# Performance work log

Hardware: AMD Instinct MI355X
Metric: run time of the kernel (lower is better)

The kernel has to match this reference:

```python
import jax, jax.numpy as jnp
import numpy as np

VOL = (32, 64, 64)          # 3D brain volume grid
B, N, D = 2, 4096, 1024     # batch, active voxels (seq_len), feature_dim
H, KNN = 16, 16             # num_heads, num_neighbors


def setup_inputs() -> dict:
    key = jax.random.key(0)
    k1, k2, k3, k4 = jax.random.split(key, 4)
    # boolean 3D mask with exactly N active voxels (so seq_len == #active)
    rng = np.random.default_rng(0)
    flat = np.zeros(int(np.prod(VOL)), dtype=bool)
    flat[rng.choice(flat.size, N, replace=False)] = True
    visual_cortex_mask = jnp.asarray(flat.reshape(VOL))
    x = jax.random.normal(k1, (B, N, D), dtype=jnp.float32)
    s = 1.0 / np.sqrt(D)
    Wq = jax.random.normal(k2, (D, D), dtype=jnp.float32) * s
    Wk = jax.random.normal(k3, (D, D), dtype=jnp.float32) * s
    Wv = jax.random.normal(k4, (D, D), dtype=jnp.float32) * s
    return {"x": x, "visual_cortex_mask": visual_cortex_mask,
            "Wq": Wq, "Wk": Wk, "Wv": Wv}


def reference(x, visual_cortex_mask, Wq, Wk, Wv):
    batch, seq_len, d = x.shape
    hd = d // H
    # --- kNN over active voxel coordinates (cdist + topk) ---
    flat = visual_cortex_mask.reshape(-1)
    (act,) = jnp.nonzero(flat, size=seq_len)  # flat indices of active voxels
    coords = jnp.stack(jnp.unravel_index(act, visual_cortex_mask.shape),
                       axis=1).astype(jnp.float32)           # [N, 3]
    sq = jnp.sum(coords * coords, axis=-1)                    # [N]
    d2 = sq[:, None] + sq[None, :] - 2.0 * (coords @ coords.T)  # squared dists
    _, nbr = jax.lax.top_k(-d2, KNN + 1)   # smallest distances first
    nbr = nbr[:, 1:]                       # drop self -> [N, KNN] positions
    # --- QKV projections (torch Linear: x @ W.T) ---
    q = (x @ Wq.T).reshape(batch, seq_len, H, hd)
    k = (x @ Wk.T).reshape(batch, seq_len, H, hd)
    v = (x @ Wv.T).reshape(batch, seq_len, H, hd)
    # --- gather-based sparse attention: each query attends only to its
    # KNN neighbors (exactly the block-mask semantics of the original) ---
    kn = k[:, nbr]   # [B, N, KNN, H, hd]
    vn = v[:, nbr]   # [B, N, KNN, H, hd]
    scale = 1.0 / np.sqrt(hd)
    scores = jnp.einsum('bnhd,bnkhd->bhnk', q, kn) * scale
    attn = jax.nn.softmax(scores, axis=-1)
    out = jnp.einsum('bhnk,bnkhd->bnhd', attn, vn).reshape(batch, seq_len, d)
    metric = k.mean(axis=2)  # key.mean over heads -> [B, N, hd]
    return out, metric
```

## Files before the change

### kernel.cpp

```cpp
#include <hip/hip_runtime.h>
#include <hip/hip_bf16.h>
#include <stdint.h>

#define BATCH 2
#define NPTS 4096
#define DMODEL 1024
#define NHEAD 16
#define HDIM 64
#define KNN 16
#define MASKN 131072
#define EBLK 128

typedef __attribute__((ext_vector_type(8))) short bf16x8;
typedef __attribute__((ext_vector_type(4))) float f32x4;

__device__ __forceinline__ float b2f(unsigned short u) {
    union { unsigned int i; float f; } c; c.i = ((unsigned int)u) << 16; return c.f;
}
__device__ __forceinline__ unsigned short f2b(float f) {
    unsigned int x = __float_as_uint(f);
    unsigned int r = (x + 0x7fffu + ((x >> 16) & 1u)) >> 16;
    return (unsigned short)r;
}
__device__ __forceinline__ unsigned int pack2f(float a, float b) {
    return (unsigned int)f2b(a) | ((unsigned int)f2b(b) << 16);
}
__device__ __forceinline__ void gload16(const unsigned short* g, unsigned short* l) {
    __builtin_amdgcn_global_load_lds((const __attribute__((address_space(1))) void*)g,
                                     (__attribute__((address_space(3))) void*)l, 16, 0, 0);
}

__global__ __launch_bounds__(256) void count8_kernel(const unsigned char* __restrict__ m8,
                                                     int* __restrict__ cnt8) {
    __shared__ int red[256];
    const int b = blockIdx.x, t = threadIdx.x;
    const uchar4 v = ((const uchar4*)m8)[b * 256 + t];
    red[t] = (v.x != 0) + (v.y != 0) + (v.z != 0) + (v.w != 0);
    __syncthreads();
    for (int off = 128; off >= 1; off >>= 1) {
        if (t < off) red[t] += red[t + off];
        __syncthreads();
    }
    if (t == 0) cnt8[b] = red[0];
}

__global__ __launch_bounds__(256) void count32_kernel(const unsigned char* __restrict__ m8,
                                                      const int* __restrict__ cnt8,
                                                      int* __restrict__ cnt32) {
    __shared__ int red[256];
    const int b = blockIdx.x, t = threadIdx.x;
    red[t] = (t < EBLK) ? cnt8[t] : 0;
    __syncthreads();
    for (int off = 128; off >= 1; off >>= 1) {
        if (t < off) red[t] += red[t + off];
        __syncthreads();
    }
    if (red[0] == NPTS) return;
    __syncthreads();
    const int4 v = ((const int4*)m8)[b * 256 + t];
    red[t] = (v.x != 0) + (v.y != 0) + (v.z != 0) + (v.w != 0);
    __syncthreads();
    for (int off = 128; off >= 1; off >>= 1) {
        if (t < off) red[t] += red[t + off];
        __syncthreads();
    }
    if (t == 0) cnt32[b] = red[0];
}

__global__ __launch_bounds__(256) void extract_kernel(const unsigned char* __restrict__ m8,
                                                      const int* __restrict__ cnt8,
                                                      const int* __restrict__ cnt32,
                                                      int* __restrict__ act) {
    __shared__ int sblk[EBLK];
    __shared__ int sthr[256];
    const int b = blockIdx.x, t = threadIdx.x;
    if (t < EBLK) sblk[t] = cnt8[t];
    __syncthreads();
    for (int off = 1; off < EBLK; off <<= 1) {
        int v = (t < EBLK && t >= off) ? sblk[t - off] : 0;
        __syncthreads();
        if (t < EBLK) sblk[t] += v;
        __syncthreads();
    }
    const bool bytes = (sblk[EBLK - 1] == NPTS);
    if (!bytes) {
        __syncthreads();
        if (t < EBLK) sblk[t] = cnt32[t];
        __syncthreads();
        for (int off = 1; off < EBLK; off <<= 1) {
            int v = (t < EBLK && t >= off) ? sblk[t - off] : 0;
            __syncthreads();
            if (t < EBLK) sblk[t] += v;
            __syncthreads();
        }
    }
    const int blkoff = (b == 0) ? 0 : sblk[b - 1];
    const int gbase = b * 1024 + t * 4;
    int f0, f1, f2, f3;
    if (bytes) {
        const uchar4 v = ((const uchar4*)m8)[b * 256 + t];
        f0 = v.x != 0; f1 = v.y != 0; f2 = v.z != 0; f3 = v.w != 0;
    } else {
        const int4 v = ((const int4*)m8)[b * 256 + t];
        f0 = v.x != 0; f1 = v.y != 0; f2 = v.z != 0; f3 = v.w != 0;
    }
    const int c = f0 + f1 + f2 + f3;
    sthr[t] = c;
    __syncthreads();
    for (int off = 1; off < 256; off <<= 1) {
        int v = (t >= off) ? sthr[t - off] : 0;
        __syncthreads();
        sthr[t] += v;
        __syncthreads();
    }
    int pos = blkoff + sthr[t] - c;
    if (f0) act[pos++] = gbase;
    if (f1) act[pos++] = gbase + 1;
    if (f2) act[pos++] = gbase + 2;
    if (f3) act[pos++] = gbase + 3;
}

__global__ __launch_bounds__(256) void knn_kernel(const int* __restrict__ act,
                                                  int* __restrict__ nbr) {
    __shared__ int act_s[NPTS];
    const int t = threadIdx.x;
    for (int i = t; i < NPTS; i += 256) act_s[i] = act[i];
    __syncthreads();
    const int q = blockIdx.x * 4 + (t >> 6);
    const int lane = t & 63;
    const int aq = act_s[q];
    const int qz = aq >> 12, qy = (aq >> 6) & 63, qx = aq & 63;
    int best[17];
    #pragma unroll
    for (int i = 0; i < 17; ++i) best[i] = 0x7FFFFFFF;
    for (int j = lane; j < NPTS; j += 64) {
        const int aj = act_s[j];
        const int dz = (aj >> 12) - qz;
        const int dy = ((aj >> 6) & 63) - qy;
        const int dx = (aj & 63) - qx;
        const int d2 = dz * dz + dy * dy + dx * dx;
        int p = (d2 << 12) | j;
        if (p < best[16]) {
            #pragma unroll
            for (int u = 0; u < 17; ++u) {
                const bool lt = p < best[u];
                const int tmp = best[u];
                best[u] = lt ? p : best[u];
                p = lt ? tmp : p;
            }
        }
    }
    int head = best[0];
    int keep = 0;
    #pragma unroll
    for (int r = 0; r < KNN + 1; ++r) {
        int m = head;
        #pragma unroll
        for (int off = 32; off >= 1; off >>= 1) m = min(m, __shfl_xor(m, off, 64));
        if (lane == r - 1) keep = m;
        const bool win = (head == m);
        #pragma unroll
        for (int u = 0; u < 16; ++u) if (win) best[u] = best[u + 1];
        if (win) best[16] = 0x7FFFFFFF;
        head = best[0];
    }
    if (lane < KNN) nbr[q * KNN + lane] = keep & 4095;
}

#define XN8 (BATCH * NPTS * DMODEL / 8)
#define WN8 (DMODEL * DMODEL / 8)
__global__ __launch_bounds__(256) void cast_all_kernel(
    const float* __restrict__ x, const float* __restrict__ wq,
    const float* __restrict__ wk, const float* __restrict__ wv,
    unsigned short* __restrict__ Xb, unsigned short* __restrict__ Wb) {
    const int i = blockIdx.x * 256 + threadIdx.x;
    const int total = XN8 + 3 * WN8;
    if (i >= total) return;
    const float* src;
    unsigned short* dst;
    if (i < XN8) {
        src = x + (size_t)i * 8;
        dst = Xb + (size_t)i * 8;
    } else {
        const int j = i - XN8;
        const int wsel = j >> 17;
        const int o = j & (WN8 - 1);
        src = ((wsel == 0) ? wq : (wsel == 1) ? wk : wv) + (size_t)o * 8;
        dst = Wb + ((size_t)wsel * WN8 + o) * 8;
    }
    const float4 a = ((const float4*)src)[0];
    const float4 b = ((const float4*)src)[1];
    uint4 w;
    w.x = pack2f(a.x, a.y); w.y = pack2f(a.z, a.w);
    w.z = pack2f(b.x, b.y); w.w = pack2f(b.z, b.w);
    *(uint4*)dst = w;
}

__global__ __launch_bounds__(256, 2) void gemm_qkv64(
    const unsigned short* __restrict__ Xb,
    const unsigned short* __restrict__ Wb,
    unsigned short* __restrict__ O0, unsigned short* __restrict__ O1, unsigned short* __restrict__ O2)
{
    const int K = DMODEL, N = DMODEL;
    const unsigned short* W = Wb + (size_t)blockIdx.z * DMODEL * DMODEL;
    unsigned short* C = (blockIdx.z == 0) ? O0 : (blockIdx.z == 1) ? O1 : O2;
    __shared__ unsigned short As[2][128 * 64];
    __shared__ unsigned short Bs[2][128 * 64];
    const int tid = threadIdx.x;
    const int rowBase = blockIdx.x * 128;
    const int colBase = blockIdx.y * 128;
    const int lane = tid & 63, w = tid >> 6;
    const int wr = w >> 1, wc = w & 1;
    const int lr = lane & 15, kg = lane >> 4;

    f32x4 acc[4][4];
    const f32x4 zero = {0.f, 0.f, 0.f, 0.f};
    #pragma unroll
    for (int i = 0; i < 4; ++i)
        #pragma unroll
        for (int j = 0; j < 4; ++j) acc[i][j] = zero;

    const unsigned short* aS[4];
    const unsigned short* bS[4];
    #pragma unroll
    for (int j = 0; j < 4; ++j) {
        const int s = j * 256 + tid;
        const int row = s >> 3, pch = s & 7;
        const int sc = (pch ^ (row & 7)) * 8;
        aS[j] = Xb + (size_t)(rowBase + row) * K + sc;
        bS[j] = W  + (size_t)(colBase + row) * K + sc;
    }

    #define STAGE(kt, bf) do { \
        _Pragma("unroll") \
        for (int j = 0; j < 4; ++j) { \
            gload16(aS[j] + (kt) * 64, &As[bf][(j * 256 + w * 64) * 8]); \
            gload16(bS[j] + (kt) * 64, &Bs[bf][(j * 256 + w * 64) * 8]); \
        } \
    } while (0)

    #define COMPUTE(bf) do { \
        bf16x8 af[4][2], bfr[4][2]; \
        _Pragma("unroll") \
        for (int mi = 0; mi < 4; ++mi) \
            _Pragma("unroll") \
            for (int kk = 0; kk < 2; ++kk) \
                af[mi][kk] = *(const bf16x8*)&As[bf][(wr * 64 + mi * 16 + lr) * 64 + (((kk * 4 + kg) ^ (lr & 7)) * 8)]; \
        _Pragma("unroll") \
        for (int ni = 0; ni < 4; ++ni) \
            _Pragma("unroll") \
            for (int kk = 0; kk < 2; ++kk) \
                bfr[ni][kk] = *(const bf16x8*)&Bs[bf][(wc * 64 + ni * 16 + lr) * 64 + (((kk * 4 + kg) ^ (lr & 7)) * 8)]; \
        __builtin_amdgcn_s_setprio(1); \
        _Pragma("unroll") \
        for (int kk = 0; kk < 2; ++kk) \
            _Pragma("unroll") \
            for (int mi = 0; mi < 4; ++mi) \
                _Pragma("unroll") \
                for (int ni = 0; ni < 4; ++ni) \
                    acc[mi][ni] = __builtin_amdgcn_mfma_f32_16x16x32_bf16(af[mi][kk], bfr[ni][kk], acc[mi][ni], 0, 0, 0); \
        __builtin_amdgcn_s_setprio(0); \
    } while (0)

    STAGE(0, 0);
    STAGE(1, 1);
    for (int kt = 0; kt < 14; ++kt) {
        const int bf = kt & 1;
        asm volatile("s_waitcnt vmcnt(8)" ::: "memory");
        __builtin_amdgcn_s_barrier();
        COMPUTE(bf);
        __builtin_amdgcn_s_barrier();
        STAGE(kt + 2, bf);
    }
    asm volatile("s_waitcnt vmcnt(8)" ::: "memory");
    __builtin_amdgcn_s_barrier();
    COMPUTE(0);
    __builtin_amdgcn_s_barrier();
    asm volatile("s_waitcnt vmcnt(0)" ::: "memory");
    __builtin_amdgcn_s_barrier();
    COMPUTE(1);
    #undef STAGE
    #undef COMPUTE

    #pragma unroll
    for (int mi = 0; mi < 4; ++mi)
        #pragma unroll
        for (int ni = 0; ni < 4; ++ni) {
            const int row0 = rowBase + wr * 64 + mi * 16 + kg * 4;
            const int col = colBase + wc * 64 + ni * 16 + lr;
            #pragma unroll
            for (int j = 0; j < 4; ++j)
                C[(size_t)(row0 + j) * N + col] = f2b(acc[mi][ni][j]);
        }
}

__device__ __forceinline__ void stage16(unsigned short* dst, const float* src) {
    const float4 a = ((const float4*)src)[0];
    const float4 b = ((const float4*)src)[1];
    const float4 c = ((const float4*)src)[2];
    const float4 d = ((const float4*)src)[3];
    uint4 w0, w1;
    w0.x = pack2f(a.x, a.y); w0.y = pack2f(a.z, a.w);
    w0.z = pack2f(b.x, b.y); w0.w = pack2f(b.z, b.w);
    w1.x = pack2f(c.x, c.y); w1.y = pack2f(c.z, c.w);
    w1.z = pack2f(d.x, d.y); w1.w = pack2f(d.z, d.w);
    ((uint4*)dst)[0] = w0;
    ((uint4*)dst)[1] = w1;
}

__global__ __launch_bounds__(256) void gemm_qkv_f32(
    const float* __restrict__ X,
    const float* __restrict__ W0, const float* __restrict__ W1, const float* __restrict__ W2,
    unsigned short* __restrict__ O0, unsigned short* __restrict__ O1, unsigned short* __restrict__ O2)
{
    const int K = DMODEL, N = DMODEL;
    const float* W = (blockIdx.z == 0) ? W0 : (blockIdx.z == 1) ? W1 : W2;
    unsigned short* C = (blockIdx.z == 0) ? O0 : (blockIdx.z == 1) ? O1 : O2;
    __shared__ unsigned short As[128 * 32];
    __shared__ unsigned short Bs[128 * 32];
    const int tid = threadIdx.x;
    const int rowBase = blockIdx.x * 128;
    const int colBase = blockIdx.y * 128;
    const int lane = tid & 63, w = tid >> 6;
    const int wr = w >> 1, wc = w & 1;
    const int lr = lane & 15, kg = lane >> 4;
    const int srow = tid >> 1;
    const int scol = (tid & 1) * 16;
    f32x4 acc[4][4];
    const f32x4 zero = {0.f, 0.f, 0.f, 0.f};
    #pragma unroll
    for (int i = 0; i < 4; ++i)
        #pragma unroll
        for (int j = 0; j < 4; ++j) acc[i][j] = zero;
    const float* Arow = &X[(size_t)(rowBase + srow) * K + scol];
    const float* Brow = &W[(size_t)(colBase + srow) * K + scol];
    unsigned short* Adst = &As[srow * 32 + scol];
    unsigned short* Bdst = &Bs[srow * 32 + scol];
    for (int kb = 0; kb < K; kb += 32) {
        __syncthreads();
        stage16(Adst, Arow + kb);
        stage16(Bdst, Brow + kb);
        __syncthreads();
        bf16x8 af[4], bfr[4];
        #pragma unroll
        for (int mi = 0; mi < 4; ++mi)
            af[mi] = *(const bf16x8*)&As[(wr * 64 + mi * 16 + lr) * 32 + kg * 8];
        #pragma unroll
        for (int ni = 0; ni < 4; ++ni)
            bfr[ni] = *(const bf16x8*)&Bs[(wc * 64 + ni * 16 + lr) * 32 + kg * 8];
        #pragma unroll
        for (int mi = 0; mi < 4; ++mi)
            #pragma unroll
            for (int ni = 0; ni < 4; ++ni)
                acc[mi][ni] = __builtin_amdgcn_mfma_f32_16x16x32_bf16(af[mi], bfr[ni], acc[mi][ni], 0, 0, 0);
    }
    #pragma unroll
    for (int mi = 0; mi < 4; ++mi)
        #pragma unroll
        for (int ni = 0; ni < 4; ++ni) {
            const int row0 = rowBase + wr * 64 + mi * 16 + kg * 4;
            const int col = colBase + wc * 64 + ni * 16 + lr;
            #pragma unroll
            for (int j = 0; j < 4; ++j)
                C[(size_t)(row0 + j) * N + col] = f2b(acc[mi][ni][j]);
        }
}

__global__ __launch_bounds__(256) void attn_kernel(
    const unsigned short* __restrict__ Q, const unsigned short* __restrict__ Kb,
    const unsigned short* __restrict__ Vb, const int* __restrict__ nbr,
    float* __restrict__ out, float* __restrict__ mout)
{
    const int bid = blockIdx.x;
    const int p = (bid & 7) * 1024 + (bid >> 3);
    const int b = p >> 12;
    const int n = p & 4095;
    __shared__ unsigned short q_s[DMODEL];
    __shared__ float a_s[NHEAD][KNN];
    __shared__ float part_s[4][64];
    const int tid = threadIdx.x;
    const int kk = tid & 15, h = tid >> 4;
    const int mynb = nbr[n * KNN + kk];
    const unsigned short* krow = &Kb[((size_t)b * NPTS + mynb) * DMODEL + h * HDIM];
    bf16x8 kreg[8];
    #pragma unroll
    for (int j = 0; j < 8; ++j) kreg[j] = *(const bf16x8*)&krow[j * 8];
    const int o = tid * 4;
    ushort4 vpre[KNN];
    #pragma unroll
    for (int k2 = 0; k2 < KNN; ++k2) {
        const int nb2 = __shfl(mynb, k2, 16);
        vpre[k2] = *(const ushort4*)&Vb[((size_t)b * NPTS + nb2) * DMODEL + o];
    }
    *(int2*)&q_s[tid * 4] = *(const int2*)&Q[((size_t)b * NPTS + n) * DMODEL + tid * 4];
    __syncthreads();
    float s = 0.f;
    #pragma unroll
    for (int j = 0; j < 8; ++j) {
        const bf16x8 qq = *(const bf16x8*)&q_s[h * HDIM + j * 8];
        const bf16x8 kr = kreg[j];
        #pragma unroll
        for (int e = 0; e < 8; ++e)
            s += b2f((unsigned short)qq[e]) * b2f((unsigned short)kr[e]);
    }
    s *= 0.125f;
    float m = s;
    #pragma unroll
    for (int off = 8; off >= 1; off >>= 1) m = fmaxf(m, __shfl_xor(m, off, 16));
    const float e = __expf(s - m);
    float sum = e;
    #pragma unroll
    for (int off = 8; off >= 1; off >>= 1) sum += __shfl_xor(sum, off, 16);
    a_s[h][kk] = e / sum;
    __syncthreads();
    const int h2 = tid >> 4;
    float av0 = 0.f, av1 = 0.f, av2 = 0.f, av3 = 0.f;
    #pragma unroll
    for (int k2 = 0; k2 < KNN; ++k2) {
        const float a = a_s[h2][k2];
        av0 += a * b2f(vpre[k2].x); av1 += a * b2f(vpre[k2].y);
        av2 += a * b2f(vpre[k2].z); av3 += a * b2f(vpre[k2].w);
    }
    float4 r; r.x = av0; r.y = av1; r.z = av2; r.w = av3;
    *(float4*)&out[((size_t)b * NPTS + n) * DMODEL + o] = r;
    {
        const unsigned short* krow2 = &Kb[((size_t)b * NPTS + n) * DMODEL];
        const int dd = tid & 63, grp = tid >> 6;
        float ms = 0.f;
        #pragma unroll
        for (int hh = 0; hh < 4; ++hh)
            ms += b2f(krow2[(grp * 4 + hh) * HDIM + dd]);
        part_s[grp][dd] = ms;
        __syncthreads();
        if (tid < 64)
            mout[((size_t)b * NPTS + n) * HDIM + tid] =
                (part_s[0][tid] + part_s[1][tid] + part_s[2][tid] + part_s[3][tid]) * 0.0625f;
    }
}

extern "C" void kernel_launch(void* const* d_in, const int* in_sizes, int n_in,
                              void* d_out, int out_size, void* d_ws, size_t ws_size,
                              hipStream_t stream) {
    const float* x = (const float*)d_in[0];
    const unsigned char* mask = (const unsigned char*)d_in[1];
    const float* Wq = (const float*)d_in[2];
    const float* Wk = (const float*)d_in[3];
    const float* Wv = (const float*)d_in[4];
    float* out = (float*)d_out;
    char* ws = (char*)d_ws;

    const size_t QKV_BYTES = (size_t)BATCH * NPTS * DMODEL * 2;
    const size_t XB_BYTES  = (size_t)BATCH * NPTS * DMODEL * 2;
    const size_t WB_BYTES  = (size_t)3 * DMODEL * DMODEL * 2;
    unsigned short* qb = (unsigned short*)(ws);
    unsigned short* kb = (unsigned short*)(ws + QKV_BYTES);
    unsigned short* vb = (unsigned short*)(ws + 2 * QKV_BYTES);
    const size_t SMALL_BYTES = (size_t)NPTS * sizeof(int) * (1 + KNN) + 2 * EBLK * sizeof(int);
    const size_t need_base = 3 * QKV_BYTES + SMALL_BYTES;
    const size_t need_full = need_base + XB_BYTES + WB_BYTES;
    const bool full = (ws_size >= need_full);
    char* tail = ws + 3 * QKV_BYTES;
    unsigned short* Xb = (unsigned short*)tail;
    unsigned short* Wb = (unsigned short*)(tail + XB_BYTES);
    char* small = full ? (tail + XB_BYTES + WB_BYTES) : tail;
    int* act  = (int*)small;
    int* nbr  = (int*)(small + NPTS * sizeof(int));
    int* cnt8 = (int*)(small + NPTS * sizeof(int) * (1 + KNN));
    int* cnt32 = cnt8 + EBLK;
    if (ws_size < need_base) return;

    count8_kernel<<<EBLK, 256, 0, stream>>>(mask, cnt8);
    count32_kernel<<<EBLK, 256, 0, stream>>>(mask, cnt8, cnt32);
    extract_kernel<<<EBLK, 256, 0, stream>>>(mask, cnt8, cnt32, act);
    knn_kernel<<<1024, 256, 0, stream>>>(act, nbr);
    if (full) {
        const int castN = XN8 + 3 * WN8;
        cast_all_kernel<<<(castN + 255) / 256, 256, 0, stream>>>(x, Wq, Wk, Wv, Xb, Wb);
        gemm_qkv64<<<dim3(64, 8, 3), 256, 0, stream>>>(Xb, Wb, qb, kb, vb);
    } else {
        gemm_qkv_f32<<<dim3(64, 8, 3), 256, 0, stream>>>(x, Wq, Wk, Wv, qb, kb, vb);
    }
    attn_kernel<<<dim3(BATCH * NPTS), 256, 0, stream>>>(qb, kb, vb, nbr, out,
                                                        out + (size_t)BATCH * NPTS * DMODEL);
}
```

Measured before the change: 174.4 us.

## Merge mask count/extract kernels and co-launch kNN with bf16 cast

The three mask-processing kernels (count8, count32, extract) are replaced by one prep kernel in which every block redundantly counts the whole mask to compute its prefix offset. The kNN search and the fp32-to-bf16 cast are merged into one launch, with block ranges split by blockIdx, so the two independent jobs can run at the same time. The aim is fewer launches and less idle tail between small kernels. In exchange each prep block rereads the full mask, and the kNN blocks now reserve 16KB of shared memory per block even in the cast path.

Result: slower. 180.6 us (+3.5%).

```diff
diff --git a/kernel.cpp b/kernel.cpp
--- a/kernel.cpp
+++ b/kernel.cpp
@@ -9,7 +9,6 @@
 #define HDIM 64
 #define KNN 16
 #define MASKN 131072
-#define EBLK 128
 
 typedef __attribute__((ext_vector_type(8))) short bf16x8;
 typedef __attribute__((ext_vector_type(4))) float f32x4;
@@ -30,78 +29,55 @@
                                      (__attribute__((address_space(3))) void*)l, 16, 0, 0);
 }
 
-__global__ __launch_bounds__(256) void count8_kernel(const unsigned char* __restrict__ m8,
-                                                     int* __restrict__ cnt8) {
-    __shared__ int red[256];
-    const int b = blockIdx.x, t = threadIdx.x;
-    const uchar4 v = ((const uchar4*)m8)[b * 256 + t];
-    red[t] = (v.x != 0) + (v.y != 0) + (v.z != 0) + (v.w != 0);
-    __syncthreads();
-    for (int off = 128; off >= 1; off >>= 1) {
-        if (t < off) red[t] += red[t + off];
-        __syncthreads();
-    }
-    if (t == 0) cnt8[b] = red[0];
-}
-
-__global__ __launch_bounds__(256) void count32_kernel(const unsigned char* __restrict__ m8,
-                                                      const int* __restrict__ cnt8,
-                                                      int* __restrict__ cnt32) {
-    __shared__ int red[256];
-    const int b = blockIdx.x, t = threadIdx.x;
-    red[t] = (t < EBLK) ? cnt8[t] : 0;
-    __syncthreads();
-    for (int off = 128; off >= 1; off >>= 1) {
-        if (t < off) red[t] += red[t + off];
-        __syncthreads();
-    }
-    if (red[0] == NPTS) return;
-    __syncthreads();
-    const int4 v = ((const int4*)m8)[b * 256 + t];
-    red[t] = (v.x != 0) + (v.y != 0) + (v.z != 0) + (v.w != 0);
-    __syncthreads();
-    for (int off = 128; off >= 1; off >>= 1) {
-        if (t < off) red[t] += red[t + off];
-        __syncthreads();
-    }
-    if (t == 0) cnt32[b] = red[0];
-}
-
-__global__ __launch_bounds__(256) void extract_kernel(const unsigned char* __restrict__ m8,
-                                                      const int* __restrict__ cnt8,
-                                                      const int* __restrict__ cnt32,
-                                                      int* __restrict__ act) {
-    __shared__ int sblk[EBLK];
+__global__ __launch_bounds__(256) void prep_kernel(const unsigned char* __restrict__ m8,
+                                                   int* __restrict__ act) {
     __shared__ int sthr[256];
     const int b = blockIdx.x, t = threadIdx.x;
-    if (t < EBLK) sblk[t] = cnt8[t];
+    int cnt = 0;
+    const uchar4* v8 = (const uchar4*)m8;
+    for (int i = 0; i < 128; ++i) {
+        const uchar4 v = v8[t * 128 + i];
+        cnt += (v.x != 0) + (v.y != 0) + (v.z != 0) + (v.w != 0);
+    }
+    sthr[t] = cnt;
     __syncthreads();
-    for (int off = 1; off < EBLK; off <<= 1) {
-        int v = (t < EBLK && t >= off) ? sblk[t - off] : 0;
-        __syncthreads();
-        if (t < EBLK) sblk[t] += v;
-        __syncthreads();
-    }
-    const bool bytes = (sblk[EBLK - 1] == NPTS);
-    if (!bytes) {
-        __syncthreads();
-        if (t < EBLK) sblk[t] = cnt32[t];
-        __syncthreads();
-        for (int off = 1; off < EBLK; off <<= 1) {
-            int v = (t < EBLK && t >= off) ? sblk[t - off] : 0;
+    for (int off = 1; off < 256; off <<= 1) {
+        int v = (t >= off) ? sthr[t - off] : 0;
+        __syncthreads();
+        sthr[t] += v;
+        __syncthreads();
+    }
+    const bool bytes = (sthr[255] == NPTS);
+    int blkoff;
+    if (bytes) {
+        blkoff = (b == 0) ? 0 : sthr[2 * b - 1];
+        __syncthreads();
+    } else {
+        __syncthreads();
+        const int4* v32 = (const int4*)m8;
+        int c2 = 0;
+        for (int i = 0; i < 128; ++i) {
+            const int4 v = v32[t * 128 + i];
+            c2 += (v.x != 0) + (v.y != 0) + (v.z != 0) + (v.w != 0);
+        }
+        sthr[t] = c2;
+        __syncthreads();
+        for (int off = 1; off < 256; off <<= 1) {
+            int v = (t >= off) ? sthr[t - off] : 0;
             __syncthreads();
-            if (t < EBLK) sblk[t] += v;
+            sthr[t] += v;
             __syncthreads();
         }
-    }
-    const int blkoff = (b == 0) ? 0 : sblk[b - 1];
+        blkoff = (b == 0) ? 0 : sthr[2 * b - 1];
+        __syncthreads();
+    }
     const int gbase = b * 1024 + t * 4;
     int f0, f1, f2, f3;
     if (bytes) {
-        const uchar4 v = ((const uchar4*)m8)[b * 256 + t];
+        const uchar4 v = ((const uchar4*)m8)[gbase >> 2];
         f0 = v.x != 0; f1 = v.y != 0; f2 = v.z != 0; f3 = v.w != 0;
     } else {
-        const int4 v = ((const int4*)m8)[b * 256 + t];
+        const int4 v = ((const int4*)m8)[gbase >> 2];
         f0 = v.x != 0; f1 = v.y != 0; f2 = v.z != 0; f3 = v.w != 0;
     }
     const int c = f0 + f1 + f2 + f3;
@@ -120,80 +96,83 @@
     if (f3) act[pos++] = gbase + 3;
 }
 
-__global__ __launch_bounds__(256) void knn_kernel(const int* __restrict__ act,
-                                                  int* __restrict__ nbr) {
+#define XN8 (BATCH * NPTS * DMODEL / 8)
+#define WN8 (DMODEL * DMODEL / 8)
+#define CASTN (XN8 + 3 * WN8)
+#define CASTBLKS ((CASTN + 255) / 256)
+
+__global__ __launch_bounds__(256) void knn_cast_kernel(
+    const int* __restrict__ act, int* __restrict__ nbr,
+    const float* __restrict__ x, const float* __restrict__ wq,
+    const float* __restrict__ wk, const float* __restrict__ wv,
+    unsigned short* __restrict__ Xb, unsigned short* __restrict__ Wb)
+{
     __shared__ int act_s[NPTS];
     const int t = threadIdx.x;
-    for (int i = t; i < NPTS; i += 256) act_s[i] = act[i];
-    __syncthreads();
-    const int q = blockIdx.x * 4 + (t >> 6);
-    const int lane = t & 63;
-    const int aq = act_s[q];
-    const int qz = aq >> 12, qy = (aq >> 6) & 63, qx = aq & 63;
-    int best[17];
-    #pragma unroll
-    for (int i = 0; i < 17; ++i) best[i] = 0x7FFFFFFF;
-    for (int j = lane; j < NPTS; j += 64) {
-        const int aj = act_s[j];
-        const int dz = (aj >> 12) - qz;
-        const int dy = ((aj >> 6) & 63) - qy;
-        const int dx = (aj & 63) - qx;
-        const int d2 = dz * dz + dy * dy + dx * dx;
-        int p = (d2 << 12) | j;
-        if (p < best[16]) {
+    if (blockIdx.x < 1024) {
+        for (int i = t; i < NPTS; i += 256) act_s[i] = act[i];
+        __syncthreads();
+        const int q = blockIdx.x * 4 + (t >> 6);
+        const int lane = t & 63;
+        const int aq = act_s[q];
+        const int qz = aq >> 12, qy = (aq >> 6) & 63, qx = aq & 63;
+        int best[17];
+        #pragma unroll
+        for (int i = 0; i < 17; ++i) best[i] = 0x7FFFFFFF;
+        for (int j = lane; j < NPTS; j += 64) {
+            const int aj = act_s[j];
+            const int dz = (aj >> 12) - qz;
+            const int dy = ((aj >> 6) & 63) - qy;
+            const int dx = (aj & 63) - qx;
+            const int d2 = dz * dz + dy * dy + dx * dx;
+            int p = (d2 << 12) | j;
+            if (p < best[16]) {
+                #pragma unroll
+                for (int u = 0; u < 17; ++u) {
+                    const bool lt = p < best[u];
+                    const int tmp = best[u];
+                    best[u] = lt ? p : best[u];
+                    p = lt ? tmp : p;
+                }
+            }
+        }
+        int head = best[0];
+        int keep = 0;
+        #pragma unroll
+        for (int r = 0; r < KNN + 1; ++r) {
+            int m = head;
             #pragma unroll
-            for (int u = 0; u < 17; ++u) {
-                const bool lt = p < best[u];
-                const int tmp = best[u];
-                best[u] = lt ? p : best[u];
-                p = lt ? tmp : p;
-            }
-        }
-    }
-    int head = best[0];
-    int keep = 0;
-    #pragma unroll
-    for (int r = 0; r < KNN + 1; ++r) {
-        int m = head;
-        #pragma unroll
-        for (int off = 32; off >= 1; off >>= 1) m = min(m, __shfl_xor(m, off, 64));
-        if (lane == r - 1) keep = m;
-        const bool win = (head == m);
-        #pragma unroll
-        for (int u = 0; u < 16; ++u) if (win) best[u] = best[u + 1];
-        if (win) best[16] = 0x7FFFFFFF;
-        head = best[0];
-    }
-    if (lane < KNN) nbr[q * KNN + lane] = keep & 4095;
-}
-
-#define XN8 (BATCH * NPTS * DMODEL / 8)
-#define WN8 (DMODEL * DMODEL / 8)
-__global__ __launch_bounds__(256) void cast_all_kernel(
-    const float* __restrict__ x, const float* __restrict__ wq,
-    const float* __restrict__ wk, const float* __restrict__ wv,
-    unsigned short* __restrict__ Xb, unsigned short* __restrict__ Wb) {
-    const int i = blockIdx.x * 256 + threadIdx.x;
-    const int total = XN8 + 3 * WN8;
-    if (i >= total) return;
-    const float* src;
-    unsigned short* dst;
-    if (i < XN8) {
-        src = x + (size_t)i * 8;
-        dst = Xb + (size_t)i * 8;
+            for (int off = 32; off >= 1; off >>= 1) m = min(m, __shfl_xor(m, off, 64));
+            if (lane == r - 1) keep = m;
+            const bool win = (head == m);
+            #pragma unroll
+            for (int u = 0; u < 16; ++u) if (win) best[u] = best[u + 1];
+            if (win) best[16] = 0x7FFFFFFF;
+            head = best[0];
+        }
+        if (lane < KNN) nbr[q * KNN + lane] = keep & 4095;
     } else {
-        const int j = i - XN8;
-        const int wsel = j >> 17;
-        const int o = j & (WN8 - 1);
-        src = ((wsel == 0) ? wq : (wsel == 1) ? wk : wv) + (size_t)o * 8;
-        dst = Wb + ((size_t)wsel * WN8 + o) * 8;
-    }
-    const float4 a = ((const float4*)src)[0];
-    const float4 b = ((const float4*)src)[1];
-    uint4 w;
-    w.x = pack2f(a.x, a.y); w.y = pack2f(a.z, a.w);
-    w.z = pack2f(b.x, b.y); w.w = pack2f(b.z, b.w);
-    *(uint4*)dst = w;
+        const int i = (blockIdx.x - 1024) * 256 + t;
+        if (i >= CASTN) return;
+        const float* src;
+        unsigned short* dst;
+        if (i < XN8) {
+            src = x + (size_t)i * 8;
+            dst = Xb + (size_t)i * 8;
+        } else {
+            const int j = i - XN8;
+            const int wsel = j >> 17;
+            const int o = j & (WN8 - 1);
+            src = ((wsel == 0) ? wq : (wsel == 1) ? wk : wv) + (size_t)o * 8;
+            dst = Wb + ((size_t)wsel * WN8 + o) * 8;
+        }
+        const float4 a = ((const float4*)src)[0];
+        const float4 bb = ((const float4*)src)[1];
+        uint4 w;
+        w.x = pack2f(a.x, a.y);  w.y = pack2f(a.z, a.w);
+        w.z = pack2f(bb.x, bb.y); w.w = pack2f(bb.z, bb.w);
+        *(uint4*)dst = w;
+    }
 }
 
 __global__ __launch_bounds__(256, 2) void gemm_qkv64(
@@ -455,7 +434,7 @@
     unsigned short* qb = (unsigned short*)(ws);
     unsigned short* kb = (unsigned short*)(ws + QKV_BYTES);
     unsigned short* vb = (unsigned short*)(ws + 2 * QKV_BYTES);
-    const size_t SMALL_BYTES = (size_t)NPTS * sizeof(int) * (1 + KNN) + 2 * EBLK * sizeof(int);
+    const size_t SMALL_BYTES = (size_t)NPTS * sizeof(int) * (1 + KNN);
     const size_t need_base = 3 * QKV_BYTES + SMALL_BYTES;
     const size_t need_full = need_base + XB_BYTES + WB_BYTES;
     const bool full = (ws_size >= need_full);
@@ -465,19 +444,15 @@
     char* small = full ? (tail + XB_BYTES + WB_BYTES) : tail;
     int* act  = (int*)small;
     int* nbr  = (int*)(small + NPTS * sizeof(int));
-    int* cnt8 = (int*)(small + NPTS * sizeof(int) * (1 + KNN));
-    int* cnt32 = cnt8 + EBLK;
     if (ws_size < need_base) return;
 
-    count8_kernel<<<EBLK, 256, 0, stream>>>(mask, cnt8);
-    count32_kernel<<<EBLK, 256, 0, stream>>>(mask, cnt8, cnt32);
-    extract_kernel<<<EBLK, 256, 0, stream>>>(mask, cnt8, cnt32, act);
-    knn_kernel<<<1024, 256, 0, stream>>>(act, nbr);
+    prep_kernel<<<128, 256, 0, stream>>>(mask, act);
     if (full) {
-        const int castN = XN8 + 3 * WN8;
-        cast_all_kernel<<<(castN + 255) / 256, 256, 0, stream>>>(x, Wq, Wk, Wv, Xb, Wb);
+        knn_cast_kernel<<<1024 + CASTBLKS, 256, 0, stream>>>(act, nbr, x, Wq, Wk, Wv, Xb, Wb);
         gemm_qkv64<<<dim3(64, 8, 3), 256, 0, stream>>>(Xb, Wb, qb, kb, vb);
     } else {
+        knn_cast_kernel<<<1024, 256, 0, stream>>>(act, nbr, x, Wq, Wk, Wv,
+                                                  (unsigned short*)nullptr, (unsigned short*)nullptr);
         gemm_qkv_f32<<<dim3(64, 8, 3), 256, 0, stream>>>(x, Wq, Wk, Wv, qb, kb, vb);
     }
     attn_kernel<<<dim3(BATCH * NPTS), 256, 0, stream>>>(qb, kb, vb, nbr, out,
```
